# Performance work log

Measured on AMD Instinct MI355X. Metric: run time of the kernel, lower is better.

## Reference

```python
import jax, jax.numpy as jnp
import numpy as np

D_MODEL = 1024
EXPAND = 2
D_INNER = D_MODEL * EXPAND  # 2048
D_STATE = 16
D_CONV = 4
DT_RANK = max(16, D_MODEL // 16)  # 64
BATCH = 1
SEQ = 2048


def _hippo_eigvals(N):
    # HiPPO-LegS matrix: A[n,m] = -(2*max(n,m)+1)
    n = np.arange(N)
    A = -(2.0 * np.maximum(n[:, None], n[None, :]) + 1.0)
    w, _ = np.linalg.eigh(A)
    idx = np.argsort(np.abs(w))[::-1]
    return w[idx]


def setup_inputs() -> dict:
    key = jax.random.key(0)
    ks = jax.random.split(key, 10)
    s = 0.02
    return {
        "x": jax.random.normal(ks[0], (BATCH, SEQ, D_MODEL), jnp.float32),
        "in_w": jax.random.normal(ks[1], (D_MODEL, D_INNER), jnp.float32) * s,
        "in_b": jnp.zeros((D_INNER,), jnp.float32),
        "conv_w": jax.random.normal(ks[2], (D_INNER, 1, D_CONV), jnp.float32) * s,
        "conv_b": jnp.zeros((D_INNER,), jnp.float32),
        "A_log": jnp.asarray(np.log(np.abs(_hippo_eigvals(D_STATE))), jnp.float32),
        "B_mat": jax.random.normal(ks[3], (D_STATE, D_INNER), jnp.float32) * s,
        "C_mat": jax.random.normal(ks[4], (D_STATE, D_INNER), jnp.float32) * s,
        "D_vec": jnp.ones((D_INNER,), jnp.float32),
        "gate_w": jax.random.normal(ks[5], (D_MODEL, D_INNER), jnp.float32) * s,
        "gate_b": jnp.zeros((D_INNER,), jnp.float32),
        "dt1_w": jax.random.normal(ks[6], (D_INNER, DT_RANK), jnp.float32) * s,
        "dt1_b": jnp.zeros((DT_RANK,), jnp.float32),
        "dt2_w": jax.random.normal(ks[7], (DT_RANK, D_INNER), jnp.float32) * s,
        "dt2_b": jnp.full((D_INNER,), -4.0, jnp.float32),  # softplus -> small dt
        "out_w": jax.random.normal(ks[8], (D_INNER, D_MODEL), jnp.float32) * s,
        "out_b": jnp.zeros((D_MODEL,), jnp.float32),
    }


def reference(x, in_w, in_b, conv_w, conv_b, A_log, B_mat, C_mat, D_vec,
              gate_w, gate_b, dt1_w, dt1_b, dt2_w, dt2_b, out_w, out_b):
    B, L, _ = x.shape
    u = x @ in_w + in_b  # (B, L, D_INNER)
    # causal depthwise conv1d: left-pad d_conv-1 (torch pads both sides then trims to L)
    uc = jax.lax.conv_general_dilated(
        u.transpose(0, 2, 1), conv_w, (1,), [(D_CONV - 1, 0)],
        dimension_numbers=("NCH", "OIH", "NCH"),
        feature_group_count=D_INNER) + conv_b[None, :, None]
    u = jax.nn.silu(uc.transpose(0, 2, 1))  # (B, L, D_INNER)
    # input-dependent time step via low-rank dt projection
    delta = jax.nn.softplus((u @ dt1_w + dt1_b) @ dt2_w + dt2_b)  # (B, L, D_INNER)
    # ZOH discretization of diagonal A (matches discretize_zoh diagonal branch)
    A = -jnp.exp(A_log)  # (N,)
    dA = delta[..., None] * A  # (B, L, D, N)
    A_bar = jnp.exp(dA)
    safe_A = jnp.where(jnp.abs(A) < 1e-6, 1.0, A)
    expansion = jnp.where(jnp.abs(A) < 1e-6,
                          delta[..., None] * (1.0 + 0.5 * dA),
                          (A_bar - 1.0) / safe_A)  # (B, L, D, N)
    Bu = expansion * B_mat.T[None, None, :, :] * u[..., None]  # (B, L, D, N)
    # sequential state recurrence h[k] = A_bar[k] * h[k-1] + B_bar[k] * u[k]
    def step(h, ab_bu):
        ab, bu = ab_bu
        h = ab * h + bu
        return h, h
    h0 = jnp.zeros((B, D_INNER, D_STATE), x.dtype)
    _, hs = jax.lax.scan(step, h0, (A_bar.transpose(1, 0, 2, 3), Bu.transpose(1, 0, 2, 3)))
    hs = hs.transpose(1, 0, 2, 3)  # (B, L, D, N)
    y = jnp.einsum("bldn,nd->bld", hs, C_mat) + D_vec * u
    y = y * jax.nn.silu(x @ gate_w + gate_b)
    return y @ out_w + out_b
```

## Files before the change

kernel.cpp:

```cpp
#include <hip/hip_runtime.h>

#define L_SEQ 2048
#define DM    1024
#define DI    2048
#define NS    16
#define DTR   64
#define CH    64
#define CL    32
#define KZ_DT 16
#define KZ_OUT 4

typedef short bf16x8_t __attribute__((ext_vector_type(8)));
typedef float f32x4    __attribute__((ext_vector_type(4)));

__device__ __forceinline__ unsigned short f2bf(float f) {
    union { float f; unsigned int u; } v; v.f = f;
    unsigned int u = v.u;
    unsigned int r = (u + 0x7FFFu + ((u >> 16) & 1u)) >> 16;
    return (unsigned short)r;
}

__global__ void cast_bf16_kernel(const float* __restrict__ in,
                                 unsigned short* __restrict__ out, int n) {
    int i = (blockIdx.x * blockDim.x + threadIdx.x) * 4;
    if (i + 3 < n) {
        float4 v = *(const float4*)&in[i];
        ushort4 o;
        o.x = f2bf(v.x); o.y = f2bf(v.y); o.z = f2bf(v.z); o.w = f2bf(v.w);
        *(ushort4*)&out[i] = o;
    }
}

__global__ void tcast_kernel(const float* __restrict__ in,
                             unsigned short* __restrict__ out, int K, int N) {
    __shared__ float tile[32][33];
    int tx = threadIdx.x & 31, ty = threadIdx.x >> 5;
    int n0 = blockIdx.x * 32, k0 = blockIdx.y * 32;
    #pragma unroll
    for (int i = ty; i < 32; i += 8) {
        int k = k0 + i, n = n0 + tx;
        tile[i][tx] = (k < K && n < N) ? in[(size_t)k * N + n] : 0.f;
    }
    __syncthreads();
    #pragma unroll
    for (int i = ty; i < 32; i += 8) {
        int n = n0 + i, k = k0 + tx;
        if (n < N && k < K) out[(size_t)n * K + k] = f2bf(tile[tx][i]);
    }
}

__global__ __launch_bounds__(256, 2)
void gemm_bf16(const unsigned short* __restrict__ A,
               const unsigned short* __restrict__ Bt,
               float* __restrict__ C,
               const float* __restrict__ bias0, const float* __restrict__ bias1,
               int bsplit, int M, int Ntot, int K, int kchunk) {
    __shared__ short As[128][40];
    __shared__ short Bs[128][40];
    const int tid  = threadIdx.x;
    const int bm   = blockIdx.y * 128, bn = blockIdx.x * 128;
    const int lane = tid & 63, wave = tid >> 6;
    const int wm   = (wave >> 1) * 64, wn = (wave & 1) * 64;
    const int quad = lane >> 4, r16 = lane & 15;

    f32x4 acc[4][4];
    #pragma unroll
    for (int i = 0; i < 4; i++)
        #pragma unroll
        for (int j = 0; j < 4; j++)
            #pragma unroll
            for (int r = 0; r < 4; r++) acc[i][j][r] = 0.f;

    const int lrow = tid >> 2;
    const int lcol = (tid & 3) * 8;
    const short* agp = (const short*)A + (size_t)(bm + lrow) * K + lcol;
    const short* bgp = (const short*)Bt + (size_t)(bn + lrow) * K + lcol;
    const size_t rstep = (size_t)64 * K;

    const int kbase  = blockIdx.z * kchunk;
    const int kiters = kchunk / 32;

    int kcur = kbase;
    bf16x8_t na0 = *(const bf16x8_t*)(agp + kcur);
    bf16x8_t na1 = *(const bf16x8_t*)(agp + rstep + kcur);
    bf16x8_t nb0 = *(const bf16x8_t*)(bgp + kcur);
    bf16x8_t nb1 = *(const bf16x8_t*)(bgp + rstep + kcur);

    for (int it = 0; it < kiters; ++it) {
        *(bf16x8_t*)&As[lrow][lcol]      = na0;
        *(bf16x8_t*)&As[lrow + 64][lcol] = na1;
        *(bf16x8_t*)&Bs[lrow][lcol]      = nb0;
        *(bf16x8_t*)&Bs[lrow + 64][lcol] = nb1;
        __syncthreads();

        int kn = (it + 1 < kiters) ? kcur + 32 : kbase;
        kcur = kn;
        na0 = *(const bf16x8_t*)(agp + kn);
        na1 = *(const bf16x8_t*)(agp + rstep + kn);
        nb0 = *(const bf16x8_t*)(bgp + kn);
        nb1 = *(const bf16x8_t*)(bgp + rstep + kn);

        bf16x8_t af[4], bfr[4];
        #pragma unroll
        for (int i = 0; i < 4; i++)
            af[i] = *(const bf16x8_t*)&As[wm + i * 16 + r16][quad * 8];
        #pragma unroll
        for (int j = 0; j < 4; j++)
            bfr[j] = *(const bf16x8_t*)&Bs[wn + j * 16 + r16][quad * 8];
        #pragma unroll
        for (int i = 0; i < 4; i++)
            #pragma unroll
            for (int j = 0; j < 4; j++)
                acc[i][j] = __builtin_amdgcn_mfma_f32_16x16x32_bf16(
                    af[i], bfr[j], acc[i][j], 0, 0, 0);
        __syncthreads();
    }

    const bool partial = (gridDim.z > 1);
    float* Cw = C + (size_t)blockIdx.z * M * Ntot;
    #pragma unroll
    for (int i = 0; i < 4; i++)
        #pragma unroll
        for (int j = 0; j < 4; j++) {
            int col = bn + wn + j * 16 + r16;
            if (col < Ntot) {
                float bv = 0.f;
                if (!partial && bias0)
                    bv = (col < bsplit) ? bias0[col] : bias1[col - bsplit];
                #pragma unroll
                for (int r = 0; r < 4; r++) {
                    int row = bm + wm + i * 16 + quad * 4 + r;
                    Cw[(size_t)row * Ntot + col] = acc[i][j][r] + bv;
                }
            }
        }
}

__global__ void reduce_out_kernel(const float* __restrict__ part,
                                  const float* __restrict__ bias,
                                  float* __restrict__ out) {
    int i = (blockIdx.x * 256 + threadIdx.x) * 4;
    int col = i & (DM - 1);
    float4 s = *(const float4*)&part[i];
    #pragma unroll
    for (int z = 1; z < KZ_OUT; z++) {
        float4 p = *(const float4*)&part[(size_t)z * L_SEQ * DM + i];
        s.x += p.x; s.y += p.y; s.z += p.z; s.w += p.w;
    }
    float4 b = *(const float4*)&bias[col];
    s.x += b.x; s.y += b.y; s.z += b.z; s.w += b.w;
    *(float4*)&out[i] = s;
}

__global__ void conv_silu_kernel(const float* __restrict__ u0,
                                 const float* __restrict__ cw,
                                 const float* __restrict__ cb,
                                 float* __restrict__ uf,
                                 unsigned short* __restrict__ ub) {
    int d = blockIdx.x * 256 + threadIdx.x;
    int l = blockIdx.y;
    float4 w = *(const float4*)&cw[d * 4];
    float wk[4] = {w.x, w.y, w.z, w.w};
    float s = cb[d];
    #pragma unroll
    for (int k = 0; k < 4; k++) {
        int ll = l - 3 + k;
        if (ll >= 0) s += u0[(size_t)ll * (2 * DI) + d] * wk[k];
    }
    float sig = 1.f / (1.f + __expf(-s));
    float v = s * sig;
    uf[(size_t)l * DI + d] = v;
    ub[(size_t)l * DI + d] = f2bf(v);
}

__global__ void delta_kernel(const float* __restrict__ dtl_part,
                             const float* __restrict__ dt1b,
                             const float* __restrict__ dt2w,
                             const float* __restrict__ dt2b,
                             float* __restrict__ delta) {
    __shared__ float dl_s[8][64];
    int tid = threadIdx.x;
    int n   = blockIdx.x * 256 + tid;
    int m0  = blockIdx.y * 8;
    for (int idx = tid; idx < 512; idx += 256) {
        int r = idx >> 6, k = idx & 63;
        float s = dt1b[k];
        #pragma unroll
        for (int z = 0; z < KZ_DT; z++)
            s += dtl_part[((size_t)z * L_SEQ + m0 + r) * DTR + k];
        dl_s[r][k] = s;
    }
    __syncthreads();
    float acc[8] = {0, 0, 0, 0, 0, 0, 0, 0};
    for (int k = 0; k < 64; k++) {
        float w = dt2w[(size_t)k * DI + n];
        #pragma unroll
        for (int r = 0; r < 8; r++) acc[r] = fmaf(dl_s[r][k], w, acc[r]);
    }
    float b = dt2b[n];
    #pragma unroll
    for (int r = 0; r < 8; r++) {
        float v = acc[r] + b;
        float sp = (v > 15.f) ? v : log1pf(__expf(v));
        delta[(size_t)(m0 + r) * DI + n] = sp;
    }
}

__global__ void scan1_kernel(const float* __restrict__ delta,
                             const float* __restrict__ uf,
                             const float* __restrict__ A_log,
                             const float* __restrict__ Bm,
                             float* __restrict__ Aprod,
                             float* __restrict__ hend) {
    int d = blockIdx.x * 256 + threadIdx.x;
    int c = blockIdx.y;
    float Av[NS], iA[NS], Bn[NS];
    bool  sm[NS];
    #pragma unroll
    for (int n = 0; n < NS; n++) {
        float a = -__expf(A_log[n]);
        Av[n] = a;
        sm[n] = fabsf(a) < 1e-6f;
        iA[n] = sm[n] ? 0.f : 1.f / a;
        Bn[n] = Bm[(size_t)n * DI + d];
    }
    float h[NS], P[NS];
    #pragma unroll
    for (int n = 0; n < NS; n++) { h[n] = 0.f; P[n] = 1.f; }
    int l0 = c * CL;
    for (int t = 0; t < CL; t++) {
        float dl = delta[(size_t)(l0 + t) * DI + d];
        float ul = uf[(size_t)(l0 + t) * DI + d];
        #pragma unroll
        for (int n = 0; n < NS; n++) {
            float dA = dl * Av[n];
            float ab = __expf(dA);
            float ex = sm[n] ? dl * fmaf(0.5f, dA, 1.f) : (ab - 1.f) * iA[n];
            float bu = ex * Bn[n] * ul;
            h[n] = fmaf(ab, h[n], bu);
            P[n] *= ab;
        }
    }
    size_t base = ((size_t)c * DI + d) * NS;
    #pragma unroll
    for (int n = 0; n < NS; n++) { Aprod[base + n] = P[n]; hend[base + n] = h[n]; }
}

__global__ void combine_kernel(const float* __restrict__ Aprod,
                               const float* __restrict__ hend,
                               float* __restrict__ carry) {
    int t = blockIdx.x * 256 + threadIdx.x;
    float h = 0.f;
    for (int c = 0; c < CH; c++) {
        size_t idx = (size_t)c * (DI * NS) + t;
        carry[idx] = h;
        h = fmaf(Aprod[idx], h, hend[idx]);
    }
}

__global__ void scan2_kernel(const float* __restrict__ delta,
                             const float* __restrict__ uf,
                             const float* __restrict__ A_log,
                             const float* __restrict__ Bm,
                             const float* __restrict__ Cm,
                             const float* __restrict__ Dv,
                             const float* __restrict__ carry,
                             float* __restrict__ ycore) {
    int d = blockIdx.x * 256 + threadIdx.x;
    int c = blockIdx.y;
    float Av[NS], iA[NS], Bn[NS], Cn[NS];
    bool  sm[NS];
    #pragma unroll
    for (int n = 0; n < NS; n++) {
        float a = -__expf(A_log[n]);
        Av[n] = a;
        sm[n] = fabsf(a) < 1e-6f;
        iA[n] = sm[n] ? 0.f : 1.f / a;
        Bn[n] = Bm[(size_t)n * DI + d];
        Cn[n] = Cm[(size_t)n * DI + d];
    }
    float Dd = Dv[d];
    size_t base = ((size_t)c * DI + d) * NS;
    float h[NS];
    #pragma unroll
    for (int n = 0; n < NS; n++) h[n] = carry[base + n];
    int l0 = c * CL;
    for (int t = 0; t < CL; t++) {
        float dl = delta[(size_t)(l0 + t) * DI + d];
        float ul = uf[(size_t)(l0 + t) * DI + d];
        float y = 0.f;
        #pragma unroll
        for (int n = 0; n < NS; n++) {
            float dA = dl * Av[n];
            float ab = __expf(dA);
            float ex = sm[n] ? dl * fmaf(0.5f, dA, 1.f) : (ab - 1.f) * iA[n];
            float bu = ex * Bn[n] * ul;
            h[n] = fmaf(ab, h[n], bu);
            y = fmaf(h[n], Cn[n], y);
        }
        ycore[(size_t)(l0 + t) * DI + d] = fmaf(Dd, ul, y);
    }
}

__global__ void gatemul_kernel(const float* __restrict__ ycore,
                               const float* __restrict__ ug,
                               unsigned short* __restrict__ yb) {
    int i = (blockIdx.x * 256 + threadIdx.x) * 4;
    int l = i >> 11, d = i & (DI - 1);
    float4 yc = *(const float4*)&ycore[i];
    float4 zr = *(const float4*)&ug[(size_t)l * (2 * DI) + DI + d];
    ushort4 o;
    o.x = f2bf(yc.x * (zr.x / (1.f + __expf(-zr.x))));
    o.y = f2bf(yc.y * (zr.y / (1.f + __expf(-zr.y))));
    o.z = f2bf(yc.z * (zr.z / (1.f + __expf(-zr.z))));
    o.w = f2bf(yc.w * (zr.w / (1.f + __expf(-zr.w))));
    *(ushort4*)&yb[i] = o;
}

extern "C" void kernel_launch(void* const* d_in, const int* in_sizes, int n_in,
                              void* d_out, int out_size, void* d_ws, size_t ws_size,
                              hipStream_t stream) {
    const float* x      = (const float*)d_in[0];
    const float* in_w   = (const float*)d_in[1];
    const float* in_b   = (const float*)d_in[2];
    const float* conv_w = (const float*)d_in[3];
    const float* conv_b = (const float*)d_in[4];
    const float* A_log  = (const float*)d_in[5];
    const float* B_mat  = (const float*)d_in[6];
    const float* C_mat  = (const float*)d_in[7];
    const float* D_vec  = (const float*)d_in[8];
    const float* gate_w = (const float*)d_in[9];
    const float* gate_b = (const float*)d_in[10];
    const float* dt1_w  = (const float*)d_in[11];
    const float* dt1_b  = (const float*)d_in[12];
    const float* dt2_w  = (const float*)d_in[13];
    const float* dt2_b  = (const float*)d_in[14];
    const float* out_w  = (const float*)d_in[15];
    const float* out_b  = (const float*)d_in[16];

    char* ws = (char*)d_ws;
    size_t off = 0;
    auto alloc = [&](size_t bytes) {
        void* p = ws + off;
        off += (bytes + 255) & ~(size_t)255;
        return p;
    };

    unsigned short* xb     = (unsigned short*)alloc((size_t)L_SEQ * DM * 2);
    unsigned short* wtig   = (unsigned short*)alloc((size_t)2 * DI * DM * 2);
    unsigned short* out_wt = (unsigned short*)alloc((size_t)DM * DI * 2);
    unsigned short* dt1_wt = (unsigned short*)alloc((size_t)128 * DI * 2);
    float* ug      = (float*)alloc((size_t)L_SEQ * 2 * DI * 4);
    unsigned short* u_bf16 = (unsigned short*)alloc((size_t)L_SEQ * DI * 2);
    float* u_f32   = (float*)alloc((size_t)L_SEQ * DI * 4);
    float* dtl_p   = (float*)alloc((size_t)KZ_DT * L_SEQ * DTR * 4);
    float* delta   = (float*)alloc((size_t)L_SEQ * DI * 4);
    float* Aprod   = (float*)alloc((size_t)CH * DI * NS * 4);
    float* hend    = (float*)alloc((size_t)CH * DI * NS * 4);
    float* carry   = (float*)alloc((size_t)CH * DI * NS * 4);
    float* ycore            = Aprod;
    unsigned short* y_bf16  = (unsigned short*)dtl_p;
    float* out_part         = ug;
    (void)ws_size; (void)in_sizes; (void)n_in; (void)out_size;

    dim3 b256(256);

    cast_bf16_kernel<<<dim3((L_SEQ * DM) / 1024), b256, 0, stream>>>(x, xb, L_SEQ * DM);
    tcast_kernel<<<dim3(DI / 32, DM / 32), b256, 0, stream>>>(in_w, wtig, DM, DI);
    tcast_kernel<<<dim3(DI / 32, DM / 32), b256, 0, stream>>>(gate_w, wtig + (size_t)DI * DM, DM, DI);
    tcast_kernel<<<dim3(DM / 32, DI / 32), b256, 0, stream>>>(out_w, out_wt, DI, DM);
    tcast_kernel<<<dim3(DTR / 32, DI / 32), b256, 0, stream>>>(dt1_w, dt1_wt, DI, DTR);

    gemm_bf16<<<dim3(2 * DI / 128, L_SEQ / 128, 1), b256, 0, stream>>>(
        xb, wtig, ug, in_b, gate_b, DI, L_SEQ, 2 * DI, DM, DM);

    conv_silu_kernel<<<dim3(DI / 256, L_SEQ), b256, 0, stream>>>(ug, conv_w, conv_b, u_f32, u_bf16);

    gemm_bf16<<<dim3(1, L_SEQ / 128, KZ_DT), b256, 0, stream>>>(
        u_bf16, dt1_wt, dtl_p, nullptr, nullptr, 0, L_SEQ, DTR, DI, DI / KZ_DT);

    delta_kernel<<<dim3(DI / 256, L_SEQ / 8), b256, 0, stream>>>(dtl_p, dt1_b, dt2_w, dt2_b, delta);

    scan1_kernel<<<dim3(DI / 256, CH), b256, 0, stream>>>(delta, u_f32, A_log, B_mat, Aprod, hend);
    combine_kernel<<<dim3((DI * NS) / 256), b256, 0, stream>>>(Aprod, hend, carry);
    scan2_kernel<<<dim3(DI / 256, CH), b256, 0, stream>>>(delta, u_f32, A_log, B_mat, C_mat, D_vec, carry, ycore);

    gatemul_kernel<<<dim3((L_SEQ * DI) / 1024), b256, 0, stream>>>(ycore, ug, y_bf16);

    gemm_bf16<<<dim3(DM / 128, L_SEQ / 128, KZ_OUT), b256, 0, stream>>>(
        y_bf16, out_wt, out_part, nullptr, nullptr, 0, L_SEQ, DM, DI, DI / KZ_OUT);
    reduce_out_kernel<<<dim3((L_SEQ * DM) / 1024), b256, 0, stream>>>(out_part, out_b, (float*)d_out);
}
```

Before: 313.7 us.

## Parallelize scan over state dim, fuse gate multiply into scan2, tile conv

The scan kernels now give each (channel, state) pair its own thread instead of one thread per channel looping over 16 states. Per-block delta and u tiles are staged in shared memory, and the C-contraction uses warp shuffles. The gate SiLU multiply and bf16 cast are fused into scan2, which removes the ycore round trip and the separate gatemul launch. The conv kernel handles 8 timesteps per thread with a sliding window, and combine uses smaller blocks to spread work over more CUs. The trade-off is more redundant exp work per thread, the added shuffle reductions, and only 1 of every 16 lanes active during the gate and write step.

```diff
diff --git a/kernel.cpp b/kernel.cpp
--- a/kernel.cpp
+++ b/kernel.cpp
@@ -157,20 +157,26 @@
                                  const float* __restrict__ cb,
                                  float* __restrict__ uf,
                                  unsigned short* __restrict__ ub) {
-    int d = blockIdx.x * 256 + threadIdx.x;
-    int l = blockIdx.y;
+    int d  = blockIdx.x * 256 + threadIdx.x;
+    int l0 = blockIdx.y * 8;
     float4 w = *(const float4*)&cw[d * 4];
-    float wk[4] = {w.x, w.y, w.z, w.w};
-    float s = cb[d];
-    #pragma unroll
-    for (int k = 0; k < 4; k++) {
-        int ll = l - 3 + k;
-        if (ll >= 0) s += u0[(size_t)ll * (2 * DI) + d] * wk[k];
-    }
-    float sig = 1.f / (1.f + __expf(-s));
-    float v = s * sig;
-    uf[(size_t)l * DI + d] = v;
-    ub[(size_t)l * DI + d] = f2bf(v);
+    float bias = cb[d];
+    float x0 = 0.f, x1 = 0.f, x2 = 0.f;
+    if (l0 >= 3) {
+        x0 = u0[(size_t)(l0 - 3) * (2 * DI) + d];
+        x1 = u0[(size_t)(l0 - 2) * (2 * DI) + d];
+        x2 = u0[(size_t)(l0 - 1) * (2 * DI) + d];
+    }
+    #pragma unroll
+    for (int t = 0; t < 8; t++) {
+        float x3 = u0[(size_t)(l0 + t) * (2 * DI) + d];
+        float s = bias + x0 * w.x + x1 * w.y + x2 * w.z + x3 * w.w;
+        float sig = 1.f / (1.f + __expf(-s));
+        float v = s * sig;
+        uf[(size_t)(l0 + t) * DI + d] = v;
+        ub[(size_t)(l0 + t) * DI + d] = f2bf(v);
+        x0 = x1; x1 = x2; x2 = x3;
+    }
 }
 
 __global__ void delta_kernel(const float* __restrict__ dtl_part,
@@ -206,50 +212,53 @@
     }
 }
 
-__global__ void scan1_kernel(const float* __restrict__ delta,
-                             const float* __restrict__ uf,
-                             const float* __restrict__ A_log,
-                             const float* __restrict__ Bm,
-                             float* __restrict__ Aprod,
-                             float* __restrict__ hend) {
-    int d = blockIdx.x * 256 + threadIdx.x;
-    int c = blockIdx.y;
-    float Av[NS], iA[NS], Bn[NS];
-    bool  sm[NS];
-    #pragma unroll
-    for (int n = 0; n < NS; n++) {
-        float a = -__expf(A_log[n]);
-        Av[n] = a;
-        sm[n] = fabsf(a) < 1e-6f;
-        iA[n] = sm[n] ? 0.f : 1.f / a;
-        Bn[n] = Bm[(size_t)n * DI + d];
-    }
-    float h[NS], P[NS];
-    #pragma unroll
-    for (int n = 0; n < NS; n++) { h[n] = 0.f; P[n] = 1.f; }
-    int l0 = c * CL;
+__global__ __launch_bounds__(256)
+void scan1_kernel(const float* __restrict__ delta,
+                  const float* __restrict__ uf,
+                  const float* __restrict__ A_log,
+                  const float* __restrict__ Bm,
+                  float* __restrict__ Aprod,
+                  float* __restrict__ hend) {
+    __shared__ float sd[CL][16];
+    __shared__ float su[CL][16];
+    const int tid = threadIdx.x;
+    const int n = tid & 15, dd = tid >> 4;
+    const int d0 = blockIdx.x * 16;
+    const int c  = blockIdx.y;
+    const int l0 = c * CL;
+    #pragma unroll
+    for (int idx = tid; idx < CL * 16; idx += 256) {
+        int t = idx >> 4, j = idx & 15;
+        sd[t][j] = delta[(size_t)(l0 + t) * DI + d0 + j];
+        su[t][j] = uf[(size_t)(l0 + t) * DI + d0 + j];
+    }
+    __syncthreads();
+    const int d = d0 + dd;
+    float a  = -__expf(A_log[n]);
+    bool  sm = fabsf(a) < 1e-6f;
+    float iA = sm ? 0.f : 1.f / a;
+    float Bn = Bm[(size_t)n * DI + d];
+    float h = 0.f, P = 1.f;
+    #pragma unroll
     for (int t = 0; t < CL; t++) {
-        float dl = delta[(size_t)(l0 + t) * DI + d];
-        float ul = uf[(size_t)(l0 + t) * DI + d];
-        #pragma unroll
-        for (int n = 0; n < NS; n++) {
-            float dA = dl * Av[n];
-            float ab = __expf(dA);
-            float ex = sm[n] ? dl * fmaf(0.5f, dA, 1.f) : (ab - 1.f) * iA[n];
-            float bu = ex * Bn[n] * ul;
-            h[n] = fmaf(ab, h[n], bu);
-            P[n] *= ab;
-        }
-    }
-    size_t base = ((size_t)c * DI + d) * NS;
-    #pragma unroll
-    for (int n = 0; n < NS; n++) { Aprod[base + n] = P[n]; hend[base + n] = h[n]; }
-}
-
-__global__ void combine_kernel(const float* __restrict__ Aprod,
-                               const float* __restrict__ hend,
-                               float* __restrict__ carry) {
-    int t = blockIdx.x * 256 + threadIdx.x;
+        float dl = sd[t][dd], ul = su[t][dd];
+        float dA = dl * a;
+        float ab = __expf(dA);
+        float ex = sm ? dl * fmaf(0.5f, dA, 1.f) : (ab - 1.f) * iA;
+        float bu = ex * Bn * ul;
+        h = fmaf(ab, h, bu);
+        P *= ab;
+    }
+    size_t base = (size_t)c * (DI * NS) + d0 * NS + tid;
+    Aprod[base] = P;
+    hend[base]  = h;
+}
+
+__global__ __launch_bounds__(64)
+void combine_kernel(const float* __restrict__ Aprod,
+                    const float* __restrict__ hend,
+                    float* __restrict__ carry) {
+    int t = blockIdx.x * 64 + threadIdx.x;
     float h = 0.f;
     for (int c = 0; c < CH; c++) {
         size_t idx = (size_t)c * (DI * NS) + t;
@@ -258,63 +267,66 @@
     }
 }
 
-__global__ void scan2_kernel(const float* __restrict__ delta,
-                             const float* __restrict__ uf,
-                             const float* __restrict__ A_log,
-                             const float* __restrict__ Bm,
-                             const float* __restrict__ Cm,
-                             const float* __restrict__ Dv,
-                             const float* __restrict__ carry,
-                             float* __restrict__ ycore) {
-    int d = blockIdx.x * 256 + threadIdx.x;
-    int c = blockIdx.y;
-    float Av[NS], iA[NS], Bn[NS], Cn[NS];
-    bool  sm[NS];
-    #pragma unroll
-    for (int n = 0; n < NS; n++) {
-        float a = -__expf(A_log[n]);
-        Av[n] = a;
-        sm[n] = fabsf(a) < 1e-6f;
-        iA[n] = sm[n] ? 0.f : 1.f / a;
-        Bn[n] = Bm[(size_t)n * DI + d];
-        Cn[n] = Cm[(size_t)n * DI + d];
-    }
+__global__ __launch_bounds__(256)
+void scan2_kernel(const float* __restrict__ delta,
+                  const float* __restrict__ uf,
+                  const float* __restrict__ ug,
+                  const float* __restrict__ A_log,
+                  const float* __restrict__ Bm,
+                  const float* __restrict__ Cm,
+                  const float* __restrict__ Dv,
+                  const float* __restrict__ carry,
+                  unsigned short* __restrict__ yb) {
+    __shared__ float sd[CL][16];
+    __shared__ float su[CL][16];
+    __shared__ float sz[CL][16];
+    __shared__ unsigned short sy[CL][16];
+    const int tid = threadIdx.x;
+    const int n = tid & 15, dd = tid >> 4;
+    const int d0 = blockIdx.x * 16;
+    const int c  = blockIdx.y;
+    const int l0 = c * CL;
+    #pragma unroll
+    for (int idx = tid; idx < CL * 16; idx += 256) {
+        int t = idx >> 4, j = idx & 15;
+        sd[t][j] = delta[(size_t)(l0 + t) * DI + d0 + j];
+        su[t][j] = uf[(size_t)(l0 + t) * DI + d0 + j];
+        sz[t][j] = ug[(size_t)(l0 + t) * (2 * DI) + DI + d0 + j];
+    }
+    __syncthreads();
+    const int d = d0 + dd;
+    float a  = -__expf(A_log[n]);
+    bool  sm = fabsf(a) < 1e-6f;
+    float iA = sm ? 0.f : 1.f / a;
+    float Bn = Bm[(size_t)n * DI + d];
+    float Cn = Cm[(size_t)n * DI + d];
     float Dd = Dv[d];
-    size_t base = ((size_t)c * DI + d) * NS;
-    float h[NS];
-    #pragma unroll
-    for (int n = 0; n < NS; n++) h[n] = carry[base + n];
-    int l0 = c * CL;
+    float h  = carry[(size_t)c * (DI * NS) + d0 * NS + tid];
+    #pragma unroll
     for (int t = 0; t < CL; t++) {
-        float dl = delta[(size_t)(l0 + t) * DI + d];
-        float ul = uf[(size_t)(l0 + t) * DI + d];
-        float y = 0.f;
-        #pragma unroll
-        for (int n = 0; n < NS; n++) {
-            float dA = dl * Av[n];
-            float ab = __expf(dA);
-            float ex = sm[n] ? dl * fmaf(0.5f, dA, 1.f) : (ab - 1.f) * iA[n];
-            float bu = ex * Bn[n] * ul;
-            h[n] = fmaf(ab, h[n], bu);
-            y = fmaf(h[n], Cn[n], y);
+        float dl = sd[t][dd], ul = su[t][dd];
+        float dA = dl * a;
+        float ab = __expf(dA);
+        float ex = sm ? dl * fmaf(0.5f, dA, 1.f) : (ab - 1.f) * iA;
+        float bu = ex * Bn * ul;
+        h = fmaf(ab, h, bu);
+        float y = h * Cn;
+        y += __shfl_xor(y, 1, 64);
+        y += __shfl_xor(y, 2, 64);
+        y += __shfl_xor(y, 4, 64);
+        y += __shfl_xor(y, 8, 64);
+        if (n == 0) {
+            float ytot = fmaf(Dd, ul, y);
+            float z = sz[t][dd];
+            float g = z / (1.f + __expf(-z));
+            sy[t][dd] = f2bf(ytot * g);
         }
-        ycore[(size_t)(l0 + t) * DI + d] = fmaf(Dd, ul, y);
-    }
-}
-
-__global__ void gatemul_kernel(const float* __restrict__ ycore,
-                               const float* __restrict__ ug,
-                               unsigned short* __restrict__ yb) {
-    int i = (blockIdx.x * 256 + threadIdx.x) * 4;
-    int l = i >> 11, d = i & (DI - 1);
-    float4 yc = *(const float4*)&ycore[i];
-    float4 zr = *(const float4*)&ug[(size_t)l * (2 * DI) + DI + d];
-    ushort4 o;
-    o.x = f2bf(yc.x * (zr.x / (1.f + __expf(-zr.x))));
-    o.y = f2bf(yc.y * (zr.y / (1.f + __expf(-zr.y))));
-    o.z = f2bf(yc.z * (zr.z / (1.f + __expf(-zr.z))));
-    o.w = f2bf(yc.w * (zr.w / (1.f + __expf(-zr.w))));
-    *(ushort4*)&yb[i] = o;
+    }
+    __syncthreads();
+    {
+        int t = tid >> 3, jj = (tid & 7) * 2;
+        *(ushort2*)&yb[(size_t)(l0 + t) * DI + d0 + jj] = *(ushort2*)&sy[t][jj];
+    }
 }
 
 extern "C" void kernel_launch(void* const* d_in, const int* in_sizes, int n_in,
@@ -358,7 +370,6 @@
     float* Aprod   = (float*)alloc((size_t)CH * DI * NS * 4);
     float* hend    = (float*)alloc((size_t)CH * DI * NS * 4);
     float* carry   = (float*)alloc((size_t)CH * DI * NS * 4);
-    float* ycore            = Aprod;
     unsigned short* y_bf16  = (unsigned short*)dtl_p;
     float* out_part         = ug;
     (void)ws_size; (void)in_sizes; (void)n_in; (void)out_size;
@@ -374,18 +385,17 @@
     gemm_bf16<<<dim3(2 * DI / 128, L_SEQ / 128, 1), b256, 0, stream>>>(
         xb, wtig, ug, in_b, gate_b, DI, L_SEQ, 2 * DI, DM, DM);
 
-    conv_silu_kernel<<<dim3(DI / 256, L_SEQ), b256, 0, stream>>>(ug, conv_w, conv_b, u_f32, u_bf16);
+    conv_silu_kernel<<<dim3(DI / 256, L_SEQ / 8), b256, 0, stream>>>(ug, conv_w, conv_b, u_f32, u_bf16);
 
     gemm_bf16<<<dim3(1, L_SEQ / 128, KZ_DT), b256, 0, stream>>>(
         u_bf16, dt1_wt, dtl_p, nullptr, nullptr, 0, L_SEQ, DTR, DI, DI / KZ_DT);
 
     delta_kernel<<<dim3(DI / 256, L_SEQ / 8), b256, 0, stream>>>(dtl_p, dt1_b, dt2_w, dt2_b, delta);
 
-    scan1_kernel<<<dim3(DI / 256, CH), b256, 0, stream>>>(delta, u_f32, A_log, B_mat, Aprod, hend);
-    combine_kernel<<<dim3((DI * NS) / 256), b256, 0, stream>>>(Aprod, hend, carry);
-    scan2_kernel<<<dim3(DI / 256, CH), b256, 0, stream>>>(delta, u_f32, A_log, B_mat, C_mat, D_vec, carry, ycore);
-
-    gatemul_kernel<<<dim3((L_SEQ * DI) / 1024), b256, 0, stream>>>(ycore, ug, y_bf16);
+    scan1_kernel<<<dim3(DI / 16, CH), b256, 0, stream>>>(delta, u_f32, A_log, B_mat, Aprod, hend);
+    combine_kernel<<<dim3((DI * NS) / 64), dim3(64), 0, stream>>>(Aprod, hend, carry);
+    scan2_kernel<<<dim3(DI / 16, CH), b256, 0, stream>>>(delta, u_f32, ug, A_log, B_mat, C_mat,
+                                                         D_vec, carry, y_bf16);
 
     gemm_bf16<<<dim3(DM / 128, L_SEQ / 128, KZ_OUT), b256, 0, stream>>>(
         y_bf16, out_wt, out_part, nullptr, nullptr, 0, L_SEQ, DM, DI, DI / KZ_OUT);
```

Result: slower. 325.1 us (+3.6%).

## Fuse gate multiply into scan, retune chunking and block sizes, register-roll conv

Applied to the files above, without the earlier changes.

The gate SiLU multiply and bf16 cast now happen inside the second scan pass, which removes the ycore round trip and one kernel launch. The chunk count doubles (CH=128, CL=16) and the scan kernels use 64-thread blocks, giving more parallel blocks in exchange for more carry traffic and a longer serial combine. The causal conv now handles 8 timesteps per thread with a rolling register window, so each input row is reloaded less often. The scan loops also prefetch the next timestep's inputs and write the state vectors as float4.

```diff
diff --git a/kernel.cpp b/kernel.cpp
--- a/kernel.cpp
+++ b/kernel.cpp
@@ -5,8 +5,8 @@
 #define DI    2048
 #define NS    16
 #define DTR   64
-#define CH    64
-#define CL    32
+#define CH    128
+#define CL    16
 #define KZ_DT 16
 #define KZ_OUT 4
 
@@ -157,20 +157,26 @@
                                  const float* __restrict__ cb,
                                  float* __restrict__ uf,
                                  unsigned short* __restrict__ ub) {
-    int d = blockIdx.x * 256 + threadIdx.x;
-    int l = blockIdx.y;
+    int d  = blockIdx.x * 256 + threadIdx.x;
+    int l0 = blockIdx.y * 8;
     float4 w = *(const float4*)&cw[d * 4];
-    float wk[4] = {w.x, w.y, w.z, w.w};
-    float s = cb[d];
-    #pragma unroll
-    for (int k = 0; k < 4; k++) {
-        int ll = l - 3 + k;
-        if (ll >= 0) s += u0[(size_t)ll * (2 * DI) + d] * wk[k];
-    }
-    float sig = 1.f / (1.f + __expf(-s));
-    float v = s * sig;
-    uf[(size_t)l * DI + d] = v;
-    ub[(size_t)l * DI + d] = f2bf(v);
+    float bias = cb[d];
+    float x0 = 0.f, x1 = 0.f, x2 = 0.f;
+    if (l0 >= 3) {
+        x0 = u0[(size_t)(l0 - 3) * (2 * DI) + d];
+        x1 = u0[(size_t)(l0 - 2) * (2 * DI) + d];
+        x2 = u0[(size_t)(l0 - 1) * (2 * DI) + d];
+    }
+    #pragma unroll
+    for (int t = 0; t < 8; t++) {
+        float x3 = u0[(size_t)(l0 + t) * (2 * DI) + d];
+        float s = bias + x0 * w.x + x1 * w.y + x2 * w.z + x3 * w.w;
+        float sig = 1.f / (1.f + __expf(-s));
+        float v = s * sig;
+        uf[(size_t)(l0 + t) * DI + d] = v;
+        ub[(size_t)(l0 + t) * DI + d] = f2bf(v);
+        x0 = x1; x1 = x2; x2 = x3;
+    }
 }
 
 __global__ void delta_kernel(const float* __restrict__ dtl_part,
@@ -206,50 +212,62 @@
     }
 }
 
-__global__ void scan1_kernel(const float* __restrict__ delta,
-                             const float* __restrict__ uf,
-                             const float* __restrict__ A_log,
-                             const float* __restrict__ Bm,
-                             float* __restrict__ Aprod,
-                             float* __restrict__ hend) {
-    int d = blockIdx.x * 256 + threadIdx.x;
-    int c = blockIdx.y;
-    float Av[NS], iA[NS], Bn[NS];
-    bool  sm[NS];
+__global__ __launch_bounds__(64)
+void scan1_kernel(const float* __restrict__ delta,
+                  const float* __restrict__ uf,
+                  const float* __restrict__ A_log,
+                  const float* __restrict__ Bm,
+                  float* __restrict__ Aprod,
+                  float* __restrict__ hend) {
+    const int d = blockIdx.x * 64 + threadIdx.x;
+    const int c = blockIdx.y;
+    const int l0 = c * CL;
+    float a[NS], iA[NS], Bn[NS];
     #pragma unroll
     for (int n = 0; n < NS; n++) {
-        float a = -__expf(A_log[n]);
-        Av[n] = a;
-        sm[n] = fabsf(a) < 1e-6f;
-        iA[n] = sm[n] ? 0.f : 1.f / a;
+        float av = -__expf(A_log[n]);
+        a[n]  = av;
+        iA[n] = (fabsf(av) < 1e-6f) ? 0.f : 1.f / av;
         Bn[n] = Bm[(size_t)n * DI + d];
     }
     float h[NS], P[NS];
     #pragma unroll
     for (int n = 0; n < NS; n++) { h[n] = 0.f; P[n] = 1.f; }
-    int l0 = c * CL;
+
+    float dl = delta[(size_t)l0 * DI + d];
+    float ul = uf[(size_t)l0 * DI + d];
+    #pragma unroll
     for (int t = 0; t < CL; t++) {
-        float dl = delta[(size_t)(l0 + t) * DI + d];
-        float ul = uf[(size_t)(l0 + t) * DI + d];
+        float dln = 0.f, uln = 0.f;
+        if (t + 1 < CL) {
+            dln = delta[(size_t)(l0 + t + 1) * DI + d];
+            uln = uf[(size_t)(l0 + t + 1) * DI + d];
+        }
         #pragma unroll
         for (int n = 0; n < NS; n++) {
-            float dA = dl * Av[n];
+            float dA = dl * a[n];
             float ab = __expf(dA);
-            float ex = sm[n] ? dl * fmaf(0.5f, dA, 1.f) : (ab - 1.f) * iA[n];
+            float ex = (fabsf(a[n]) < 1e-6f) ? dl * fmaf(0.5f, dA, 1.f)
+                                             : (ab - 1.f) * iA[n];
             float bu = ex * Bn[n] * ul;
             h[n] = fmaf(ab, h[n], bu);
             P[n] *= ab;
         }
+        dl = dln; ul = uln;
     }
     size_t base = ((size_t)c * DI + d) * NS;
     #pragma unroll
-    for (int n = 0; n < NS; n++) { Aprod[base + n] = P[n]; hend[base + n] = h[n]; }
-}
-
-__global__ void combine_kernel(const float* __restrict__ Aprod,
-                               const float* __restrict__ hend,
-                               float* __restrict__ carry) {
-    int t = blockIdx.x * 256 + threadIdx.x;
+    for (int q = 0; q < 4; q++) {
+        *(float4*)&Aprod[base + q * 4] = make_float4(P[q*4], P[q*4+1], P[q*4+2], P[q*4+3]);
+        *(float4*)&hend[base + q * 4]  = make_float4(h[q*4], h[q*4+1], h[q*4+2], h[q*4+3]);
+    }
+}
+
+__global__ __launch_bounds__(64)
+void combine_kernel(const float* __restrict__ Aprod,
+                    const float* __restrict__ hend,
+                    float* __restrict__ carry) {
+    int t = blockIdx.x * 64 + threadIdx.x;
     float h = 0.f;
     for (int c = 0; c < CH; c++) {
         size_t idx = (size_t)c * (DI * NS) + t;
@@ -258,63 +276,63 @@
     }
 }
 
-__global__ void scan2_kernel(const float* __restrict__ delta,
-                             const float* __restrict__ uf,
-                             const float* __restrict__ A_log,
-                             const float* __restrict__ Bm,
-                             const float* __restrict__ Cm,
-                             const float* __restrict__ Dv,
-                             const float* __restrict__ carry,
-                             float* __restrict__ ycore) {
-    int d = blockIdx.x * 256 + threadIdx.x;
-    int c = blockIdx.y;
-    float Av[NS], iA[NS], Bn[NS], Cn[NS];
-    bool  sm[NS];
+__global__ __launch_bounds__(64)
+void scan2_kernel(const float* __restrict__ delta,
+                  const float* __restrict__ uf,
+                  const float* __restrict__ ug,
+                  const float* __restrict__ A_log,
+                  const float* __restrict__ Bm,
+                  const float* __restrict__ Cm,
+                  const float* __restrict__ Dv,
+                  const float* __restrict__ carry,
+                  unsigned short* __restrict__ yb) {
+    const int d = blockIdx.x * 64 + threadIdx.x;
+    const int c = blockIdx.y;
+    const int l0 = c * CL;
+    float a[NS], iA[NS], Bn[NS], Cn[NS], h[NS];
     #pragma unroll
     for (int n = 0; n < NS; n++) {
-        float a = -__expf(A_log[n]);
-        Av[n] = a;
-        sm[n] = fabsf(a) < 1e-6f;
-        iA[n] = sm[n] ? 0.f : 1.f / a;
+        float av = -__expf(A_log[n]);
+        a[n]  = av;
+        iA[n] = (fabsf(av) < 1e-6f) ? 0.f : 1.f / av;
         Bn[n] = Bm[(size_t)n * DI + d];
         Cn[n] = Cm[(size_t)n * DI + d];
     }
     float Dd = Dv[d];
-    size_t base = ((size_t)c * DI + d) * NS;
-    float h[NS];
-    #pragma unroll
-    for (int n = 0; n < NS; n++) h[n] = carry[base + n];
-    int l0 = c * CL;
+    size_t cbase = ((size_t)c * DI + d) * NS;
+    #pragma unroll
+    for (int q = 0; q < 4; q++) {
+        float4 cv = *(const float4*)&carry[cbase + q * 4];
+        h[q*4] = cv.x; h[q*4+1] = cv.y; h[q*4+2] = cv.z; h[q*4+3] = cv.w;
+    }
+
+    float dl = delta[(size_t)l0 * DI + d];
+    float ul = uf[(size_t)l0 * DI + d];
+    float zr = ug[(size_t)l0 * (2 * DI) + DI + d];
+    #pragma unroll
     for (int t = 0; t < CL; t++) {
-        float dl = delta[(size_t)(l0 + t) * DI + d];
-        float ul = uf[(size_t)(l0 + t) * DI + d];
+        float dln = 0.f, uln = 0.f, zrn = 0.f;
+        if (t + 1 < CL) {
+            dln = delta[(size_t)(l0 + t + 1) * DI + d];
+            uln = uf[(size_t)(l0 + t + 1) * DI + d];
+            zrn = ug[(size_t)(l0 + t + 1) * (2 * DI) + DI + d];
+        }
         float y = 0.f;
         #pragma unroll
         for (int n = 0; n < NS; n++) {
-            float dA = dl * Av[n];
+            float dA = dl * a[n];
             float ab = __expf(dA);
-            float ex = sm[n] ? dl * fmaf(0.5f, dA, 1.f) : (ab - 1.f) * iA[n];
+            float ex = (fabsf(a[n]) < 1e-6f) ? dl * fmaf(0.5f, dA, 1.f)
+                                             : (ab - 1.f) * iA[n];
             float bu = ex * Bn[n] * ul;
             h[n] = fmaf(ab, h[n], bu);
             y = fmaf(h[n], Cn[n], y);
         }
-        ycore[(size_t)(l0 + t) * DI + d] = fmaf(Dd, ul, y);
-    }
-}
-
-__global__ void gatemul_kernel(const float* __restrict__ ycore,
-                               const float* __restrict__ ug,
-                               unsigned short* __restrict__ yb) {
-    int i = (blockIdx.x * 256 + threadIdx.x) * 4;
-    int l = i >> 11, d = i & (DI - 1);
-    float4 yc = *(const float4*)&ycore[i];
-    float4 zr = *(const float4*)&ug[(size_t)l * (2 * DI) + DI + d];
-    ushort4 o;
-    o.x = f2bf(yc.x * (zr.x / (1.f + __expf(-zr.x))));
-    o.y = f2bf(yc.y * (zr.y / (1.f + __expf(-zr.y))));
-    o.z = f2bf(yc.z * (zr.z / (1.f + __expf(-zr.z))));
-    o.w = f2bf(yc.w * (zr.w / (1.f + __expf(-zr.w))));
-    *(ushort4*)&yb[i] = o;
+        float ytot = fmaf(Dd, ul, y);
+        float g = zr / (1.f + __expf(-zr));
+        yb[(size_t)(l0 + t) * DI + d] = f2bf(ytot * g);
+        dl = dln; ul = uln; zr = zrn;
+    }
 }
 
 extern "C" void kernel_launch(void* const* d_in, const int* in_sizes, int n_in,
@@ -358,7 +376,6 @@
     float* Aprod   = (float*)alloc((size_t)CH * DI * NS * 4);
     float* hend    = (float*)alloc((size_t)CH * DI * NS * 4);
     float* carry   = (float*)alloc((size_t)CH * DI * NS * 4);
-    float* ycore            = Aprod;
     unsigned short* y_bf16  = (unsigned short*)dtl_p;
     float* out_part         = ug;
     (void)ws_size; (void)in_sizes; (void)n_in; (void)out_size;
@@ -374,18 +391,17 @@
     gemm_bf16<<<dim3(2 * DI / 128, L_SEQ / 128, 1), b256, 0, stream>>>(
         xb, wtig, ug, in_b, gate_b, DI, L_SEQ, 2 * DI, DM, DM);
 
-    conv_silu_kernel<<<dim3(DI / 256, L_SEQ), b256, 0, stream>>>(ug, conv_w, conv_b, u_f32, u_bf16);
+    conv_silu_kernel<<<dim3(DI / 256, L_SEQ / 8), b256, 0, stream>>>(ug, conv_w, conv_b, u_f32, u_bf16);
 
     gemm_bf16<<<dim3(1, L_SEQ / 128, KZ_DT), b256, 0, stream>>>(
         u_bf16, dt1_wt, dtl_p, nullptr, nullptr, 0, L_SEQ, DTR, DI, DI / KZ_DT);
 
     delta_kernel<<<dim3(DI / 256, L_SEQ / 8), b256, 0, stream>>>(dtl_p, dt1_b, dt2_w, dt2_b, delta);
 
-    scan1_kernel<<<dim3(DI / 256, CH), b256, 0, stream>>>(delta, u_f32, A_log, B_mat, Aprod, hend);
-    combine_kernel<<<dim3((DI * NS) / 256), b256, 0, stream>>>(Aprod, hend, carry);
-    scan2_kernel<<<dim3(DI / 256, CH), b256, 0, stream>>>(delta, u_f32, A_log, B_mat, C_mat, D_vec, carry, ycore);
-
-    gatemul_kernel<<<dim3((L_SEQ * DI) / 1024), b256, 0, stream>>>(ycore, ug, y_bf16);
+    scan1_kernel<<<dim3(DI / 64, CH), dim3(64), 0, stream>>>(delta, u_f32, A_log, B_mat, Aprod, hend);
+    combine_kernel<<<dim3((DI * NS) / 64), dim3(64), 0, stream>>>(Aprod, hend, carry);
+    scan2_kernel<<<dim3(DI / 64, CH), dim3(64), 0, stream>>>(delta, u_f32, ug, A_log, B_mat, C_mat,
+                                                             D_vec, carry, y_bf16);
 
     gemm_bf16<<<dim3(DM / 128, L_SEQ / 128, KZ_OUT), b256, 0, stream>>>(
         y_bf16, out_wt, out_part, nullptr, nullptr, 0, L_SEQ, DM, DI, DI / KZ_OUT);
```

After: 290.1 us. 7.5% less time.
